# Optimization experiments

Hardware: AMD Instinct MI355X
Metric: run time of the kernel (lower is better)

Reference implementation:

```python
import jax, jax.numpy as jnp
import numpy as np

N_NODES = 100000
D = 128          # out_channels
H = 128          # hidden_dim
N_EDGES = 1000000


def setup_inputs() -> dict:
    key = jax.random.key(0)
    k_z, k_e, k_w1, k_b1, k_w2, k_b2 = jax.random.split(key, 6)
    z = jax.random.normal(k_z, (N_NODES, D), dtype=jnp.float32)
    edge_label_index = jax.random.randint(k_e, (2, N_EDGES), 0, N_NODES, dtype=jnp.int64)
    # nn.Linear default init: U(-1/sqrt(fan_in), 1/sqrt(fan_in))
    lim1 = 1.0 / np.sqrt(2 * D)
    lim2 = 1.0 / np.sqrt(H)
    W1 = jax.random.uniform(k_w1, (2 * D, H), jnp.float32, -lim1, lim1)
    b1 = jax.random.uniform(k_b1, (H,), jnp.float32, -lim1, lim1)
    W2 = jax.random.uniform(k_w2, (H, 1), jnp.float32, -lim2, lim2)
    b2 = jax.random.uniform(k_b2, (1,), jnp.float32, -lim2, lim2)
    return {"z": z, "edge_label_index": edge_label_index,
            "W1": W1, "b1": b1, "W2": W2, "b2": b2}


def reference(z, edge_label_index, W1, b1, W2, b2):
    src = edge_label_index[0]
    dst = edge_label_index[1]
    # gather + concat -> [n_edges, 2D]
    edge_feat = jnp.concatenate([z[src], z[dst]], axis=-1)
    h = jax.nn.relu(edge_feat @ W1 + b1)        # [n_edges, H]
    out = (h @ W2 + b2).squeeze(-1)             # [n_edges]
    return out
```

## Files before the change

kernel.cpp:

```cpp
#include <hip/hip_runtime.h>
#include <hip/hip_fp16.h>

typedef _Float16 half_t;
typedef __attribute__((ext_vector_type(2))) _Float16 f16x2;
typedef __attribute__((ext_vector_type(4))) _Float16 f16x4;
typedef __attribute__((ext_vector_type(8))) _Float16 f16x8;
typedef __attribute__((ext_vector_type(4))) float f32x4;


__global__ void prep_kernel(const float* __restrict__ z,
                            const float* __restrict__ W1,
                            half_t* __restrict__ zh,
                            half_t* __restrict__ w1s, int n8) {
    if (blockIdx.x < 128) {
        const int t = blockIdx.x * 256 + threadIdx.x;
        const int j  = t & 7;
        const int L  = (t >> 3) & 63;
        const int nt = (t >> 9) & 15;
        const int ks = t >> 13;
        const int k    = ks * 32 + (L >> 4) * 8 + j;
        const int ncol = nt * 16 + (L & 15);
        const int row  = (ncol < 128) ? k : 128 + k;
        w1s[t] = (half_t)W1[row * 128 + (ncol & 127)];
    } else {
        const int t = (blockIdx.x - 128) * 256 + threadIdx.x;
        if (t < n8) {
            const float4 a = reinterpret_cast<const float4*>(z)[2 * t];
            const float4 b = reinterpret_cast<const float4*>(z)[2 * t + 1];
            f16x8 o;
            o[0] = (_Float16)a.x; o[1] = (_Float16)a.y;
            o[2] = (_Float16)a.z; o[3] = (_Float16)a.w;
            o[4] = (_Float16)b.x; o[5] = (_Float16)b.y;
            o[6] = (_Float16)b.z; o[7] = (_Float16)b.w;
            reinterpret_cast<f16x8*>(zh)[t] = o;
        }
    }
}

__global__ __launch_bounds__(256, 3)
void gemm_regb_kernel(const half_t* __restrict__ zh,
                      const half_t* __restrict__ w1s,
                      half_t* __restrict__ Y,
                      int n_groups, int stride_groups) {
    const int wq   = threadIdx.x >> 6;
    const int lane = threadIdx.x & 63;
    const int nlo  = lane & 15;
    const int quad = lane >> 4;

    const f16x8* blob = reinterpret_cast<const f16x8*>(w1s);
    f16x8 breg[4][4];
#pragma unroll
    for (int ks = 0; ks < 4; ++ks)
#pragma unroll
        for (int ntp = 0; ntp < 4; ++ntp)
            breg[ks][ntp] = blob[(ks * 16 + wq * 4 + ntp) * 64 + lane];

    int g = blockIdx.x;
    if (g >= n_groups) return;

    const half_t* arow = zh + ((size_t)(g * 16 + nlo) * 128) + quad * 8;
    f16x8 av[4];
#pragma unroll
    for (int ks = 0; ks < 4; ++ks)
        av[ks] = *reinterpret_cast<const f16x8*>(arow + ks * 32);

    for (; g < n_groups; g += stride_groups) {
        const int gn = g + stride_groups;
        const int gpi = (gn < n_groups) ? gn : g;
        const half_t* arow_n = zh + ((size_t)(gpi * 16 + nlo) * 128) + quad * 8;
        f16x8 avn[4];
#pragma unroll
        for (int ks = 0; ks < 4; ++ks)
            avn[ks] = *reinterpret_cast<const f16x8*>(arow_n + ks * 32);

        f32x4 acc[4];
#pragma unroll
        for (int ntp = 0; ntp < 4; ++ntp) acc[ntp] = (f32x4){0.f, 0.f, 0.f, 0.f};

#pragma unroll
        for (int ks = 0; ks < 4; ++ks)
#pragma unroll
            for (int ntp = 0; ntp < 4; ++ntp)
                acc[ntp] = __builtin_amdgcn_mfma_f32_16x16x32_f16(
                    av[ks], breg[ks][ntp], acc[ntp], 0, 0, 0);

#pragma unroll
        for (int r = 0; r < 4; ++r) {
            const int nr = g * 16 + quad * 4 + r;
            f16x4 o;
#pragma unroll
            for (int j = 0; j < 4; ++j) o[j] = (_Float16)acc[j][r];
            *reinterpret_cast<f16x4*>(Y + (size_t)nr * 256 + wq * 64 +
                                      nlo * 4) = o;
        }

#pragma unroll
        for (int ks = 0; ks < 4; ++ks) av[ks] = avn[ks];
    }
}

static __device__ __forceinline__ f16x2 pair2(const f16x8& v, int p) {
    f16x2 r; r[0] = v[2 * p]; r[1] = v[2 * p + 1]; return r;
}

__global__ __launch_bounds__(256, 8)
void edge_decode_kernel(const half_t* __restrict__ Y,
                        const int* __restrict__ es,
                        const int* __restrict__ ed,
                        const float* __restrict__ b1,
                        const float* __restrict__ W2,
                        const float* __restrict__ b2,
                        float* __restrict__ out,
                        int n_e, int stride_e) {
    __shared__ __align__(16) half_t b1h[128];
    __shared__ __align__(16) half_t w2h[128];
    if (threadIdx.x < 128) {
        const int i = threadIdx.x;
        const int n = (((i >> 6) << 2) + (i & 3)) * 16 + ((i >> 2) & 15);
        b1h[i] = (half_t)b1[n];
        w2h[i] = (half_t)W2[n];
    }
    __syncthreads();

    const int lane  = threadIdx.x & 63;
    const int sl    = lane & 15;
    const int eslot = lane >> 4;
    const f16x8 bv = reinterpret_cast<const f16x8*>(b1h)[sl];
    const f16x8 wv = reinterpret_cast<const f16x8*>(w2h)[sl];
    const float b2v = b2[0];
    const f16x2 zero2 = {(_Float16)0, (_Float16)0};

    const int w = blockIdx.x * 4 + (threadIdx.x >> 6);
    int e0 = w * 4;
    if (e0 >= n_e) return;

    int ec = e0 + eslot; if (ec >= n_e) ec = 0;
    int sa = es[ec], da = ed[ec];
    f16x8 u0 = *reinterpret_cast<const f16x8*>(Y + (size_t)sa * 256 + sl * 8);
    f16x8 v0 = *reinterpret_cast<const f16x8*>(Y + (size_t)da * 256 + 128 +
                                               sl * 8);
    ec = e0 + stride_e + eslot; if (ec >= n_e) ec = 0;
    sa = es[ec]; da = ed[ec];
    f16x8 u1 = *reinterpret_cast<const f16x8*>(Y + (size_t)sa * 256 + sl * 8);
    f16x8 v1 = *reinterpret_cast<const f16x8*>(Y + (size_t)da * 256 + 128 +
                                               sl * 8);
    ec = e0 + 2 * stride_e + eslot; if (ec >= n_e) ec = 0;
    int s2 = es[ec], d2 = ed[ec];

    for (; e0 < n_e; e0 += stride_e) {
        const int e = e0 + eslot;
        const bool valid = (e < n_e);

        const f16x8 u2 = *reinterpret_cast<const f16x8*>(
            Y + (size_t)s2 * 256 + sl * 8);
        const f16x8 v2 = *reinterpret_cast<const f16x8*>(
            Y + (size_t)d2 * 256 + 128 + sl * 8);

        {
            int en = e0 + 3 * stride_e + eslot;
            if (en >= n_e) en = 0;
            s2 = es[en];
            d2 = ed[en];
        }

        float acc = 0.f;
#pragma unroll
        for (int p = 0; p < 4; ++p) {
            f16x2 h2 = pair2(u0, p) + pair2(v0, p) + pair2(bv, p);
            h2 = __builtin_elementwise_max(h2, zero2);
            acc = __builtin_amdgcn_fdot2(h2, pair2(wv, p), acc, false);
        }
        acc += __shfl_xor(acc, 1);
        acc += __shfl_xor(acc, 2);
        acc += __shfl_xor(acc, 4);
        acc += __shfl_xor(acc, 8);
        if (sl == 0 && valid) out[e] = acc + b2v;

        u0 = u1; v0 = v1;
        u1 = u2; v1 = v2;
    }
}

__global__ void naive_edge_kernel(const float* __restrict__ z,
                                  const int* __restrict__ eidx,
                                  const float* __restrict__ W1,
                                  const float* __restrict__ b1,
                                  const float* __restrict__ W2,
                                  const float* __restrict__ b2,
                                  float* __restrict__ out, int n_edges) {
    __shared__ float feat[256];
    __shared__ float red[2];
    const int e = blockIdx.x;
    const int t = threadIdx.x;
    const int s = eidx[e], d = eidx[n_edges + e];
    feat[t] = z[(size_t)s * 128 + t];
    feat[128 + t] = z[(size_t)d * 128 + t];
    __syncthreads();
    float h = b1[t];
    for (int k = 0; k < 256; ++k) h = fmaf(feat[k], W1[k * 128 + t], h);
    float p = fmaxf(h, 0.f) * W2[t];
    for (int off = 32; off; off >>= 1) p += __shfl_down(p, off);
    if ((t & 63) == 0) red[t >> 6] = p;
    __syncthreads();
    if (t == 0) out[e] = red[0] + red[1] + b2[0];
}

extern "C" void kernel_launch(void* const* d_in, const int* in_sizes, int n_in,
                              void* d_out, int out_size, void* d_ws,
                              size_t ws_size, hipStream_t stream) {
    const float* z   = (const float*)d_in[0];
    const int* eidx  = (const int*)d_in[1];
    const float* W1  = (const float*)d_in[2];
    const float* b1  = (const float*)d_in[3];
    const float* W2  = (const float*)d_in[4];
    const float* b2  = (const float*)d_in[5];
    float* out       = (float*)d_out;

    const int nz      = in_sizes[0];
    const int n_nodes = nz / 128;
    const int n_edges = in_sizes[1] / 2;

    const size_t Y_bytes   = (size_t)n_nodes * 256 * sizeof(half_t);
    const size_t zh_bytes  = (size_t)nz * sizeof(half_t);
    const size_t w1s_bytes = 32768 * sizeof(half_t);

    if (ws_size >= Y_bytes + zh_bytes + w1s_bytes) {
        half_t* Y   = (half_t*)d_ws;
        half_t* zh  = (half_t*)((char*)d_ws + Y_bytes);
        half_t* w1s = (half_t*)((char*)d_ws + Y_bytes + zh_bytes);

        const int n8 = nz / 8;
        const int zblocks = (n8 + 255) / 256;
        prep_kernel<<<128 + zblocks, 256, 0, stream>>>(z, W1, zh, w1s, n8);

        const int n_groups = n_nodes / 16;
        const int gblocks  = 1024;
        gemm_regb_kernel<<<gblocks, 256, 0, stream>>>(zh, w1s, Y, n_groups,
                                                      gblocks);

        const int eblocks  = 2048;
        const int stride_e = eblocks * 4 * 4;
        const int nq = 4;
        int qbase = 0;
        for (int q = 0; q < nq; ++q) {
            const int qlen = n_edges / nq + (q < (n_edges % nq) ? 1 : 0);
            edge_decode_kernel<<<eblocks, 256, 0, stream>>>(
                Y, eidx + qbase, eidx + n_edges + qbase, b1, W2, b2,
                out + qbase, qlen, stride_e);
            qbase += qlen;
        }
    } else {
        naive_edge_kernel<<<n_edges, 128, 0, stream>>>(z, eidx, W1, b1, W2, b2,
                                                       out, n_edges);
    }
}
```

Baseline: 195.6 us.

## Fuse fp32-to-fp16 conversion into GEMM and merge edge decode launches

Removes the separate prep kernel: the GEMM now reads fp32 z and W1 directly and converts to fp16 in registers, so the fp16 copy of z is no longer written and re-read. The four quarter-sized edge decode launches are merged into one, and the GEMM grid drops from 1024 to 768 blocks. In exchange, each block does a strided, uncoalesced load of W1 with per-element conversion, and it moves twice as many bytes of z per row, which raises register pressure in the prefetch loop.

```diff
diff --git a/kernel.cpp b/kernel.cpp
--- a/kernel.cpp
+++ b/kernel.cpp
@@ -8,74 +8,69 @@
 typedef __attribute__((ext_vector_type(4))) float f32x4;
 
 
-__global__ void prep_kernel(const float* __restrict__ z,
-                            const float* __restrict__ W1,
-                            half_t* __restrict__ zh,
-                            half_t* __restrict__ w1s, int n8) {
-    if (blockIdx.x < 128) {
-        const int t = blockIdx.x * 256 + threadIdx.x;
-        const int j  = t & 7;
-        const int L  = (t >> 3) & 63;
-        const int nt = (t >> 9) & 15;
-        const int ks = t >> 13;
-        const int k    = ks * 32 + (L >> 4) * 8 + j;
-        const int ncol = nt * 16 + (L & 15);
-        const int row  = (ncol < 128) ? k : 128 + k;
-        w1s[t] = (half_t)W1[row * 128 + (ncol & 127)];
-    } else {
-        const int t = (blockIdx.x - 128) * 256 + threadIdx.x;
-        if (t < n8) {
-            const float4 a = reinterpret_cast<const float4*>(z)[2 * t];
-            const float4 b = reinterpret_cast<const float4*>(z)[2 * t + 1];
-            f16x8 o;
-            o[0] = (_Float16)a.x; o[1] = (_Float16)a.y;
-            o[2] = (_Float16)a.z; o[3] = (_Float16)a.w;
-            o[4] = (_Float16)b.x; o[5] = (_Float16)b.y;
-            o[6] = (_Float16)b.z; o[7] = (_Float16)b.w;
-            reinterpret_cast<f16x8*>(zh)[t] = o;
-        }
-    }
-}
-
 __global__ __launch_bounds__(256, 3)
-void gemm_regb_kernel(const half_t* __restrict__ zh,
-                      const half_t* __restrict__ w1s,
-                      half_t* __restrict__ Y,
-                      int n_groups, int stride_groups) {
+void gemm_fused_kernel(const float* __restrict__ z,
+                       const float* __restrict__ W1,
+                       half_t* __restrict__ Y,
+                       int n_groups, int stride_groups) {
     const int wq   = threadIdx.x >> 6;
     const int lane = threadIdx.x & 63;
     const int nlo  = lane & 15;
     const int quad = lane >> 4;
 
-    const f16x8* blob = reinterpret_cast<const f16x8*>(w1s);
+    const int rbase = (wq >= 2) ? 128 : 0;
     f16x8 breg[4][4];
 #pragma unroll
     for (int ks = 0; ks < 4; ++ks)
 #pragma unroll
-        for (int ntp = 0; ntp < 4; ++ntp)
-            breg[ks][ntp] = blob[(ks * 16 + wq * 4 + ntp) * 64 + lane];
+        for (int ntp = 0; ntp < 4; ++ntp) {
+            const int col  = (wq & 1) * 64 + ntp * 16 + nlo;
+            const int row0 = rbase + ks * 32 + quad * 8;
+            f16x8 b;
+#pragma unroll
+            for (int j = 0; j < 8; ++j)
+                b[j] = (_Float16)W1[(row0 + j) * 128 + col];
+            breg[ks][ntp] = b;
+        }
 
     int g = blockIdx.x;
     if (g >= n_groups) return;
 
-    const half_t* arow = zh + ((size_t)(g * 16 + nlo) * 128) + quad * 8;
+    const float4* ap = reinterpret_cast<const float4*>(
+        z + ((size_t)(g * 16 + nlo) * 128) + quad * 8);
+    float4 af[4][2];
+#pragma unroll
+    for (int ks = 0; ks < 4; ++ks) {
+        af[ks][0] = ap[ks * 8];
+        af[ks][1] = ap[ks * 8 + 1];
+    }
     f16x8 av[4];
 #pragma unroll
-    for (int ks = 0; ks < 4; ++ks)
-        av[ks] = *reinterpret_cast<const f16x8*>(arow + ks * 32);
+    for (int ks = 0; ks < 4; ++ks) {
+        f16x8 t;
+        t[0] = (_Float16)af[ks][0].x; t[1] = (_Float16)af[ks][0].y;
+        t[2] = (_Float16)af[ks][0].z; t[3] = (_Float16)af[ks][0].w;
+        t[4] = (_Float16)af[ks][1].x; t[5] = (_Float16)af[ks][1].y;
+        t[6] = (_Float16)af[ks][1].z; t[7] = (_Float16)af[ks][1].w;
+        av[ks] = t;
+    }
 
     for (; g < n_groups; g += stride_groups) {
         const int gn = g + stride_groups;
         const int gpi = (gn < n_groups) ? gn : g;
-        const half_t* arow_n = zh + ((size_t)(gpi * 16 + nlo) * 128) + quad * 8;
-        f16x8 avn[4];
-#pragma unroll
-        for (int ks = 0; ks < 4; ++ks)
-            avn[ks] = *reinterpret_cast<const f16x8*>(arow_n + ks * 32);
+        const float4* apn = reinterpret_cast<const float4*>(
+            z + ((size_t)(gpi * 16 + nlo) * 128) + quad * 8);
+        float4 afn[4][2];
+#pragma unroll
+        for (int ks = 0; ks < 4; ++ks) {
+            afn[ks][0] = apn[ks * 8];
+            afn[ks][1] = apn[ks * 8 + 1];
+        }
 
         f32x4 acc[4];
 #pragma unroll
-        for (int ntp = 0; ntp < 4; ++ntp) acc[ntp] = (f32x4){0.f, 0.f, 0.f, 0.f};
+        for (int ntp = 0; ntp < 4; ++ntp)
+            acc[ntp] = (f32x4){0.f, 0.f, 0.f, 0.f};
 
 #pragma unroll
         for (int ks = 0; ks < 4; ++ks)
@@ -95,7 +90,14 @@
         }
 
 #pragma unroll
-        for (int ks = 0; ks < 4; ++ks) av[ks] = avn[ks];
+        for (int ks = 0; ks < 4; ++ks) {
+            f16x8 t;
+            t[0] = (_Float16)afn[ks][0].x; t[1] = (_Float16)afn[ks][0].y;
+            t[2] = (_Float16)afn[ks][0].z; t[3] = (_Float16)afn[ks][0].w;
+            t[4] = (_Float16)afn[ks][1].x; t[5] = (_Float16)afn[ks][1].y;
+            t[6] = (_Float16)afn[ks][1].z; t[7] = (_Float16)afn[ks][1].w;
+            av[ks] = t;
+        }
     }
 }
 
@@ -220,35 +222,20 @@
     const int n_nodes = nz / 128;
     const int n_edges = in_sizes[1] / 2;
 
-    const size_t Y_bytes   = (size_t)n_nodes * 256 * sizeof(half_t);
-    const size_t zh_bytes  = (size_t)nz * sizeof(half_t);
-    const size_t w1s_bytes = 32768 * sizeof(half_t);
-
-    if (ws_size >= Y_bytes + zh_bytes + w1s_bytes) {
-        half_t* Y   = (half_t*)d_ws;
-        half_t* zh  = (half_t*)((char*)d_ws + Y_bytes);
-        half_t* w1s = (half_t*)((char*)d_ws + Y_bytes + zh_bytes);
-
-        const int n8 = nz / 8;
-        const int zblocks = (n8 + 255) / 256;
-        prep_kernel<<<128 + zblocks, 256, 0, stream>>>(z, W1, zh, w1s, n8);
+    const size_t Y_bytes = (size_t)n_nodes * 256 * sizeof(half_t);
+
+    if (ws_size >= Y_bytes) {
+        half_t* Y = (half_t*)d_ws;
 
         const int n_groups = n_nodes / 16;
-        const int gblocks  = 1024;
-        gemm_regb_kernel<<<gblocks, 256, 0, stream>>>(zh, w1s, Y, n_groups,
-                                                      gblocks);
+        const int gblocks  = 768;
+        gemm_fused_kernel<<<gblocks, 256, 0, stream>>>(z, W1, Y, n_groups,
+                                                       gblocks);
 
         const int eblocks  = 2048;
         const int stride_e = eblocks * 4 * 4;
-        const int nq = 4;
-        int qbase = 0;
-        for (int q = 0; q < nq; ++q) {
-            const int qlen = n_edges / nq + (q < (n_edges % nq) ? 1 : 0);
-            edge_decode_kernel<<<eblocks, 256, 0, stream>>>(
-                Y, eidx + qbase, eidx + n_edges + qbase, b1, W2, b2,
-                out + qbase, qlen, stride_e);
-            qbase += qlen;
-        }
+        edge_decode_kernel<<<eblocks, 256, 0, stream>>>(
+            Y, eidx, eidx + n_edges, b1, W2, b2, out, n_edges, stride_e);
     } else {
         naive_edge_kernel<<<n_edges, 128, 0, stream>>>(z, eidx, W1, b1, W2, b2,
                                                        out, n_edges);
```

Result: no change. 194.7 us (-0.5%).

## Fuse fp32-to-fp16 conversion of z into GEMM via double-buffered LDS

Applied to the files above, without the earlier changes.

The separate pass that wrote a half-precision copy of z is removed. The per-node GEMM now reads fp32 z directly, converts it in registers, and stages it in a swizzled, double-buffered shared-memory tile with a barrier each iteration. The GEMM grid drops from 1024 to 768 blocks, and the edge decoder runs as one launch instead of four. This saves one full read/write round trip of z plus kernel launches, at the cost of LDS traffic and per-iteration block synchronisation in the GEMM.

```diff
diff --git a/kernel.cpp b/kernel.cpp
--- a/kernel.cpp
+++ b/kernel.cpp
@@ -8,42 +8,29 @@
 typedef __attribute__((ext_vector_type(4))) float f32x4;
 
 
-__global__ void prep_kernel(const float* __restrict__ z,
-                            const float* __restrict__ W1,
-                            half_t* __restrict__ zh,
-                            half_t* __restrict__ w1s, int n8) {
-    if (blockIdx.x < 128) {
-        const int t = blockIdx.x * 256 + threadIdx.x;
-        const int j  = t & 7;
-        const int L  = (t >> 3) & 63;
-        const int nt = (t >> 9) & 15;
-        const int ks = t >> 13;
-        const int k    = ks * 32 + (L >> 4) * 8 + j;
-        const int ncol = nt * 16 + (L & 15);
-        const int row  = (ncol < 128) ? k : 128 + k;
-        w1s[t] = (half_t)W1[row * 128 + (ncol & 127)];
-    } else {
-        const int t = (blockIdx.x - 128) * 256 + threadIdx.x;
-        if (t < n8) {
-            const float4 a = reinterpret_cast<const float4*>(z)[2 * t];
-            const float4 b = reinterpret_cast<const float4*>(z)[2 * t + 1];
-            f16x8 o;
-            o[0] = (_Float16)a.x; o[1] = (_Float16)a.y;
-            o[2] = (_Float16)a.z; o[3] = (_Float16)a.w;
-            o[4] = (_Float16)b.x; o[5] = (_Float16)b.y;
-            o[6] = (_Float16)b.z; o[7] = (_Float16)b.w;
-            reinterpret_cast<f16x8*>(zh)[t] = o;
-        }
-    }
+__global__ void prep_w1_kernel(const float* __restrict__ W1,
+                               half_t* __restrict__ w1s) {
+    const int t = blockIdx.x * 256 + threadIdx.x;
+    const int j  = t & 7;
+    const int L  = (t >> 3) & 63;
+    const int nt = (t >> 9) & 15;
+    const int ks = t >> 13;
+    const int k    = ks * 32 + (L >> 4) * 8 + j;
+    const int ncol = nt * 16 + (L & 15);
+    const int row  = (ncol < 128) ? k : 128 + k;
+    w1s[t] = (half_t)W1[row * 128 + (ncol & 127)];
 }
 
 __global__ __launch_bounds__(256, 3)
-void gemm_regb_kernel(const half_t* __restrict__ zh,
-                      const half_t* __restrict__ w1s,
-                      half_t* __restrict__ Y,
-                      int n_groups, int stride_groups) {
-    const int wq   = threadIdx.x >> 6;
-    const int lane = threadIdx.x & 63;
+void gemm_all_kernel(const float* __restrict__ z,
+                     const half_t* __restrict__ w1s,
+                     half_t* __restrict__ Y,
+                     int n_groups, int stride_groups) {
+    __shared__ __align__(16) half_t abuf[2][2048];
+
+    const int tid  = threadIdx.x;
+    const int wq   = tid >> 6;
+    const int lane = tid & 63;
     const int nlo  = lane & 15;
     const int quad = lane >> 4;
 
@@ -55,27 +42,45 @@
         for (int ntp = 0; ntp < 4; ++ntp)
             breg[ks][ntp] = blob[(ks * 16 + wq * 4 + ntp) * 64 + lane];
 
+    const int sr    = tid & 15;
+    const int sslot = tid >> 4;
+    const int swz_w = (sslot ^ (sr & 7)) * 8 + sr * 128;
+
     int g = blockIdx.x;
-    if (g >= n_groups) return;
-
-    const half_t* arow = zh + ((size_t)(g * 16 + nlo) * 128) + quad * 8;
-    f16x8 av[4];
-#pragma unroll
-    for (int ks = 0; ks < 4; ++ks)
-        av[ks] = *reinterpret_cast<const f16x8*>(arow + ks * 32);
-
+
+    {
+        const float4* ap = reinterpret_cast<const float4*>(
+            z + ((size_t)(g * 16 + sr) * 128) + sslot * 8);
+        const float4 a0 = ap[0];
+        const float4 a1 = ap[1];
+        f16x8 w;
+        w[0] = (_Float16)a0.x; w[1] = (_Float16)a0.y;
+        w[2] = (_Float16)a0.z; w[3] = (_Float16)a0.w;
+        w[4] = (_Float16)a1.x; w[5] = (_Float16)a1.y;
+        w[6] = (_Float16)a1.z; w[7] = (_Float16)a1.w;
+        *reinterpret_cast<f16x8*>(&abuf[0][swz_w]) = w;
+    }
+    __syncthreads();
+
+    int cur = 0;
     for (; g < n_groups; g += stride_groups) {
-        const int gn = g + stride_groups;
+        const int gn  = g + stride_groups;
         const int gpi = (gn < n_groups) ? gn : g;
-        const half_t* arow_n = zh + ((size_t)(gpi * 16 + nlo) * 128) + quad * 8;
-        f16x8 avn[4];
+        const float4* apn = reinterpret_cast<const float4*>(
+            z + ((size_t)(gpi * 16 + sr) * 128) + sslot * 8);
+        const float4 a0 = apn[0];
+        const float4 a1 = apn[1];
+
+        f16x8 av[4];
 #pragma unroll
         for (int ks = 0; ks < 4; ++ks)
-            avn[ks] = *reinterpret_cast<const f16x8*>(arow_n + ks * 32);
+            av[ks] = *reinterpret_cast<const f16x8*>(
+                &abuf[cur][nlo * 128 + (((quad + 4 * ks) ^ (nlo & 7)) << 3)]);
 
         f32x4 acc[4];
 #pragma unroll
-        for (int ntp = 0; ntp < 4; ++ntp) acc[ntp] = (f32x4){0.f, 0.f, 0.f, 0.f};
+        for (int ntp = 0; ntp < 4; ++ntp)
+            acc[ntp] = (f32x4){0.f, 0.f, 0.f, 0.f};
 
 #pragma unroll
         for (int ks = 0; ks < 4; ++ks)
@@ -94,8 +99,16 @@
                                       nlo * 4) = o;
         }
 
-#pragma unroll
-        for (int ks = 0; ks < 4; ++ks) av[ks] = avn[ks];
+        {
+            f16x8 w;
+            w[0] = (_Float16)a0.x; w[1] = (_Float16)a0.y;
+            w[2] = (_Float16)a0.z; w[3] = (_Float16)a0.w;
+            w[4] = (_Float16)a1.x; w[5] = (_Float16)a1.y;
+            w[6] = (_Float16)a1.z; w[7] = (_Float16)a1.w;
+            *reinterpret_cast<f16x8*>(&abuf[cur ^ 1][swz_w]) = w;
+        }
+        __syncthreads();
+        cur ^= 1;
     }
 }
 
@@ -221,34 +234,23 @@
     const int n_edges = in_sizes[1] / 2;
 
     const size_t Y_bytes   = (size_t)n_nodes * 256 * sizeof(half_t);
-    const size_t zh_bytes  = (size_t)nz * sizeof(half_t);
     const size_t w1s_bytes = 32768 * sizeof(half_t);
 
-    if (ws_size >= Y_bytes + zh_bytes + w1s_bytes) {
+    if (ws_size >= Y_bytes + w1s_bytes) {
         half_t* Y   = (half_t*)d_ws;
-        half_t* zh  = (half_t*)((char*)d_ws + Y_bytes);
-        half_t* w1s = (half_t*)((char*)d_ws + Y_bytes + zh_bytes);
-
-        const int n8 = nz / 8;
-        const int zblocks = (n8 + 255) / 256;
-        prep_kernel<<<128 + zblocks, 256, 0, stream>>>(z, W1, zh, w1s, n8);
+        half_t* w1s = (half_t*)((char*)d_ws + Y_bytes);
+
+        prep_w1_kernel<<<128, 256, 0, stream>>>(W1, w1s);
 
         const int n_groups = n_nodes / 16;
-        const int gblocks  = 1024;
-        gemm_regb_kernel<<<gblocks, 256, 0, stream>>>(zh, w1s, Y, n_groups,
-                                                      gblocks);
+        const int gblocks  = 768;
+        gemm_all_kernel<<<gblocks, 256, 0, stream>>>(z, w1s, Y, n_groups,
+                                                     gblocks);
 
         const int eblocks  = 2048;
         const int stride_e = eblocks * 4 * 4;
-        const int nq = 4;
-        int qbase = 0;
-        for (int q = 0; q < nq; ++q) {
-            const int qlen = n_edges / nq + (q < (n_edges % nq) ? 1 : 0);
-            edge_decode_kernel<<<eblocks, 256, 0, stream>>>(
-                Y, eidx + qbase, eidx + n_edges + qbase, b1, W2, b2,
-                out + qbase, qlen, stride_e);
-            qbase += qlen;
-        }
+        edge_decode_kernel<<<eblocks, 256, 0, stream>>>(
+            Y, eidx, eidx + n_edges, b1, W2, b2, out, n_edges, stride_e);
     } else {
         naive_edge_kernel<<<n_edges, 128, 0, stream>>>(z, eidx, W1, b1, W2, b2,
                                                        out, n_edges);
```

Result: faster. 178.6 us (-8.7%).
